# Optimization experiments

Hardware: AMD Instinct MI355X
Metric: run time of the kernel (lower is better)

Reference implementation:

```python
import jax, jax.numpy as jnp
import numpy as np

B, L, D, N_HEADS = 4, 8192, 1024, 16
HD = D // N_HEADS
MASK_NEG = -1e10


def setup_inputs() -> dict:
    key = jax.random.key(0)
    ks = jax.random.split(key, 5)
    # xavier_normal std for square Dense: sqrt(2/(fan_in+fan_out))
    std = (2.0 / (D + D)) ** 0.5
    return {
        "query": jax.random.normal(ks[0], (B, L, D), dtype=jnp.float32),
        "mask": jax.random.bernoulli(ks[1], 0.1, (B, L)),  # True = masked out
        "Wq": std * jax.random.normal(ks[2], (D, D), dtype=jnp.float32),
        "bq": jnp.zeros((D,), dtype=jnp.float32),
        "Wk": std * jax.random.normal(ks[3], (D, D), dtype=jnp.float32),
        "bk": jnp.zeros((D,), dtype=jnp.float32),
        "Wv": std * jax.random.normal(ks[4], (D, D), dtype=jnp.float32),
        "bv": jnp.zeros((D,), dtype=jnp.float32),
    }


def reference(query, mask, Wq, bq, Wk, bk, Wv, bv):
    # Self-attention: key = value = query (original falls back when key/value are None)
    q = query @ Wq + bq  # [B, L, D]
    k = query @ Wk + bk
    v = query @ Wv + bv
    # split heads: b l (n h) -> b l n h
    qs = q.reshape(B, L, N_HEADS, HD)
    ks_ = k.reshape(B, L, N_HEADS, HD)
    vs = v.reshape(B, L, N_HEADS, HD)
    m = mask[:, :, None, None]  # [B, L, 1, 1], broadcast over heads & dims
    K = jnp.where(m, MASK_NEG, ks_)
    V = jnp.where(m, 0.0, vs)
    # elu kernel feature map: phi(x) = elu(x) + 1 (elu(-1e10)+1 -> 0 for masked keys)
    phiK = jax.nn.elu(K) + 1.0
    phiQ = jax.nn.elu(qs) + 1.0
    # per-head kv summary: [B, N, HD_k, HD_v]
    kv = jnp.einsum('blnk,blnv->bnkv', phiK, V)
    # FAITHFUL to original einsum 'blk,bkv->blk': sums kv over v, elementwise with phiQ
    kv_sum = kv.sum(-1)  # [B, N, HD]
    out = phiQ * kv_sum[:, None, :, :]  # [B, L, N, HD]
    # combine heads: b l n h -> b l (n h)
    return out.reshape(B, L, D)
```

## Files before the change

### kernel.cpp

```cpp
#include <hip/hip_runtime.h>

typedef unsigned short u16;
typedef unsigned int u32;
typedef __attribute__((ext_vector_type(8))) short s16x8;
typedef __attribute__((ext_vector_type(4))) float f32x4;

#define GAS __attribute__((address_space(1)))
#define LAS __attribute__((address_space(3)))

#define BB 4
#define LL 8192
#define DD 1024
#define NH 16
#define HD 64
#define MROWS (BB * LL)
#define NWBT 2064

__device__ __forceinline__ u16 f2bf(float f) {
  u32 u = __builtin_bit_cast(u32, f);
  u32 r = (u + 0x7FFFu + ((u >> 16) & 1u)) >> 16;
  return (u16)r;
}
__device__ __forceinline__ float bf2f(u32 lo) {
  return __builtin_bit_cast(float, lo << 16);
}

__device__ __forceinline__ void async16(const void* g, void* l) {
  __builtin_amdgcn_global_load_lds((const GAS u32*)g, (LAS u32*)l, 16, 0, 0);
}

__device__ __forceinline__ bool get_mask(const void* mp, int row, int mode) {
  if (mode == 2) return ((const unsigned char*)mp)[row] != 0;
  if (mode == 1) return ((const float*)mp)[row] != 0.f;
  return ((const int*)mp)[row] != 0;
}

__global__ void build_wbt(const float* __restrict__ Wq, const float* __restrict__ Wk,
                          u16* __restrict__ WbT) {
  __shared__ float t[32][33];
  const int n0 = blockIdx.x * 32;
  const int k0 = blockIdx.y * 32;
  const float* W = (n0 >> 10) == 0 ? Wq : Wk;
  const int nloc = n0 & 1023;
  const int tx = threadIdx.x, ty = threadIdx.y;
#pragma unroll
  for (int j = 0; j < 32; j += 8)
    t[ty + j][tx] = W[(size_t)(k0 + ty + j) * DD + nloc + tx];
  __syncthreads();
#pragma unroll
  for (int j = 0; j < 32; j += 8)
    WbT[(size_t)(n0 + ty + j) * DD + k0 + tx] = f2bf(t[tx][ty + j]);
}

__global__ void build_aux(const float* __restrict__ Wv, const float* __restrict__ bq,
                          const float* __restrict__ bk, const float* __restrict__ bv,
                          const u32* __restrict__ m,
                          u16* __restrict__ WbT, float* __restrict__ bcat,
                          int* __restrict__ flag) {
  const int blk = blockIdx.x;
  const int tid = threadIdx.x;
  if (blk < 64) {
    int i = blk * 256 + tid;
    int k = i >> 4, h = i & 15;
    float s = 0.f;
    const float* p = Wv + (size_t)k * DD + h * HD;
#pragma unroll 8
    for (int j = 0; j < 64; ++j) s += p[j];
    WbT[(size_t)(2048 + h) * DD + k] = f2bf(s);
  } else if (blk < 73) {
    int i = (blk - 64) * 256 + tid;
    if (i < 1024) bcat[i] = bq[i];
    else if (i < 2048) bcat[i] = bk[i - 1024];
    else if (i < 2064) {
      float s = 0.f;
      const float* p = bv + (i - 2048) * HD;
#pragma unroll 8
      for (int j = 0; j < 64; ++j) s += p[j];
      bcat[i] = s;
    }
  } else {
    int i = (blk - 73) * 256 + tid;
    u32 v = m[i];
    int f = 0;
    if (v == 0x3F800000u) f = 1;
    else if (v > 1u) f = 2;
    if (f) atomicMax(flag, f);
  }
}

__global__ __launch_bounds__(256) void prep_q(
    const float* __restrict__ query, const u16* __restrict__ WbT,
    const float* __restrict__ bcat, const void* __restrict__ maskp,
    const int* __restrict__ mmode,
    u16* __restrict__ qb, float* __restrict__ sV) {
  __shared__ float sVp[2][16][16];
  const int tid = threadIdx.x;
  const int lane = tid & 63;
  const int w = tid >> 6;
  const int wl = w >> 1;
  const int ks = w & 1;
  const int l15 = lane & 15, l16 = lane >> 4;
  const int row0 = blockIdx.x * 32 + wl * 16;
  const int arow = row0 + l15;

  const float* qrow = query + (size_t)arow * DD + ks * 512 + l16 * 8;
  u16* qbrow = qb + (size_t)arow * DD + ks * 512 + l16 * 8;
  const u16* wrow = WbT + (size_t)(2048 + l15) * DD + ks * 512 + l16 * 8;

  f32x4 acc = {};
#pragma unroll
  for (int mac = 0; mac < 2; ++mac) {
    float4 qv[16];
    s16x8 wv[8];
#pragma unroll
    for (int s = 0; s < 8; ++s) {
      const int off = mac * 256 + s * 32;
      qv[s * 2] = *(const float4*)(qrow + off);
      qv[s * 2 + 1] = *(const float4*)(qrow + off + 4);
      wv[s] = *(const s16x8*)(wrow + off);
    }
#pragma unroll
    for (int s = 0; s < 8; ++s) {
      s16x8 o;
      o[0] = (short)f2bf(qv[s * 2].x);     o[1] = (short)f2bf(qv[s * 2].y);
      o[2] = (short)f2bf(qv[s * 2].z);     o[3] = (short)f2bf(qv[s * 2].w);
      o[4] = (short)f2bf(qv[s * 2 + 1].x); o[5] = (short)f2bf(qv[s * 2 + 1].y);
      o[6] = (short)f2bf(qv[s * 2 + 1].z); o[7] = (short)f2bf(qv[s * 2 + 1].w);
      *(s16x8*)(qbrow + mac * 256 + s * 32) = o;
      acc = __builtin_amdgcn_mfma_f32_16x16x32_bf16(o, wv[s], acc, 0, 0, 0);
    }
  }

  if (ks == 1) {
#pragma unroll
    for (int r = 0; r < 4; ++r) sVp[wl][l16 * 4 + r][l15] = acc[r];
  }
  __syncthreads();
  if (ks == 0) {
    const int mode = *mmode;
#pragma unroll
    for (int r = 0; r < 4; ++r) {
      const int row = row0 + l16 * 4 + r;
      const bool msk = get_mask(maskp, row, mode);
      float v = acc[r] + sVp[wl][l16 * 4 + r][l15] + bcat[2048 + l15];
      sV[(size_t)row * NH + l15] = msk ? 0.f : v;
    }
  }
}

#define AOFF(buf) ((buf) * 4096)
#define BOFF(buf) (8192 + (buf) * 16384)

__global__ __launch_bounds__(512, 2) void gemm_qkv(
    const u16* __restrict__ qb, const u16* __restrict__ WbT,
    const float* __restrict__ bcat, const void* __restrict__ maskp,
    const int* __restrict__ mmode,
    const float* __restrict__ sV, float* __restrict__ kv,
    float* __restrict__ out, int phase) {
  __shared__ __align__(16) u16 lds[40960];
  const int tid = threadIdx.x;
  const int lane = tid & 63;
  const int w = tid >> 6;
  const int wm = w & 1, wn = w >> 1;
  const int l15 = lane & 15, l16 = lane >> 4;

  const int bid = blockIdx.x;
  const int swz = (bid & 7) * 64 + (bid >> 3);
  const int mt = swz >> 1;
  const int nt = swz & 1;
  const int row0 = mt * 128;
  const int col0 = (phase ? 1024 : 0) + nt * 512;

  f32x4 acc[4][8] = {};

#define STAGE_A(buf, kt) do {                                               \
    int row_ = tid >> 2, slot_ = tid & 3;                                   \
    int c_ = slot_ ^ ((row_ >> 1) & 3);                                     \
    async16(qb + (size_t)(row0 + row_) * DD + (kt) * 32 + c_ * 8,           \
            lds + AOFF(buf) + tid * 8);                                     \
  } while (0)

#define STAGE_B(buf, kt) do {                                               \
    _Pragma("unroll")                                                       \
    for (int j_ = 0; j_ < 4; ++j_) {                                        \
      int li_ = tid + j_ * 512;                                             \
      int row_ = li_ >> 2, slot_ = li_ & 3;                                 \
      int c_ = slot_ ^ ((row_ >> 1) & 3);                                   \
      async16(WbT + (size_t)(col0 + row_) * DD + (kt) * 32 + c_ * 8,        \
              lds + BOFF(buf) + li_ * 8);                                   \
    }                                                                       \
  } while (0)

#define LDA(buf, a) do {                                                    \
    _Pragma("unroll")                                                       \
    for (int mi_ = 0; mi_ < 4; ++mi_) {                                     \
      int r_ = wm * 64 + mi_ * 16 + l15;                                    \
      a[mi_] = *(const s16x8*)(lds + AOFF(buf) + r_ * 32 +                  \
                               ((l16 ^ ((r_ >> 1) & 3)) * 8));              \
    }                                                                       \
  } while (0)

#define LDB4(buf, nb, b) do {                                               \
    _Pragma("unroll")                                                       \
    for (int q_ = 0; q_ < 4; ++q_) {                                        \
      int r_ = wn * 128 + (nb) * 64 + q_ * 16 + l15;                        \
      b[q_] = *(const s16x8*)(lds + BOFF(buf) + r_ * 32 +                   \
                              ((l16 ^ ((r_ >> 1) & 3)) * 8));               \
    }                                                                       \
  } while (0)

#define MM(a, b, nb) do {                                                   \
    __builtin_amdgcn_s_setprio(1);                                          \
    _Pragma("unroll")                                                       \
    for (int mi_ = 0; mi_ < 4; ++mi_) {                                     \
      _Pragma("unroll")                                                     \
      for (int q_ = 0; q_ < 4; ++q_) {                                      \
        acc[mi_][(nb)*4 + q_] = __builtin_amdgcn_mfma_f32_16x16x32_bf16(    \
            a[mi_], b[q_], acc[mi_][(nb)*4 + q_], 0, 0, 0);                 \
      }                                                                     \
    }                                                                       \
    __builtin_amdgcn_s_setprio(0);                                          \
  } while (0)

#define BAR() __builtin_amdgcn_s_barrier()
#define VMW1() asm volatile("s_waitcnt vmcnt(1)" ::: "memory")
#define VMW5() asm volatile("s_waitcnt vmcnt(5)" ::: "memory")
#define VMW0() asm volatile("s_waitcnt vmcnt(0)" ::: "memory")

  STAGE_A(0, 0); STAGE_B(0, 0); STAGE_A(1, 1); STAGE_B(1, 1);
  VMW5();
  BAR();

  for (int t = 0; t < 30; t += 2) {
    s16x8 a[4], b[4];
    LDA(0, a); LDB4(0, 0, b);
    if (t > 0) STAGE_B(1, t + 1);
    BAR(); MM(a, b, 0); BAR();
    LDB4(0, 1, b);
    STAGE_A(0, t + 2);
    BAR(); MM(a, b, 1); VMW1(); BAR();
    LDA(1, a); LDB4(1, 0, b);
    STAGE_B(0, t + 2);
    BAR(); MM(a, b, 0); BAR();
    LDB4(1, 1, b);
    STAGE_A(1, t + 3);
    BAR(); MM(a, b, 1); VMW1(); BAR();
  }

  {
    s16x8 a[4], b[4];
    LDA(0, a); LDB4(0, 0, b);
    STAGE_B(1, 31);
    BAR(); MM(a, b, 0); BAR();
    LDB4(0, 1, b);
    BAR(); MM(a, b, 1); VMW0(); BAR();
    LDA(1, a); LDB4(1, 0, b);
    BAR(); MM(a, b, 0); BAR();
    LDB4(1, 1, b);
    BAR(); MM(a, b, 1);
  }

  const int mode = *mmode;
  const int lanec = lane & 15, laneq = lane >> 4;
  const int wcol0 = col0 + wn * 128;
  const int b_ = row0 >> 13;

  if (phase == 1) {
    const int h0 = (wcol0 - 1024) >> 6;
    float pc[8] = {0.f, 0.f, 0.f, 0.f, 0.f, 0.f, 0.f, 0.f};
#pragma unroll
    for (int mi = 0; mi < 4; ++mi) {
#pragma unroll
      for (int r = 0; r < 4; ++r) {
        const int row = row0 + wm * 64 + mi * 16 + laneq * 4 + r;
        const bool msk = get_mask(maskp, row, mode);
        if (!msk) {
          const float sv0 = sV[(size_t)row * NH + h0];
          const float sv1 = sV[(size_t)row * NH + h0 + 1];
#pragma unroll
          for (int nj = 0; nj < 8; ++nj) {
            const int col = wcol0 + nj * 16 + lanec;
            float v = acc[mi][nj][r] + bcat[col];
            float phi = v > 0.f ? v + 1.f : __expf(v);
            pc[nj] += phi * (nj < 4 ? sv0 : sv1);
          }
        }
      }
    }
#pragma unroll
    for (int nj = 0; nj < 8; ++nj) {
      pc[nj] += __shfl_xor(pc[nj], 16);
      pc[nj] += __shfl_xor(pc[nj], 32);
    }
    if (laneq == 0) {
#pragma unroll
      for (int nj = 0; nj < 8; ++nj) {
        const int colk = wcol0 - 1024 + nj * 16 + lanec;
        atomicAdd(&kv[b_ * DD + colk], pc[nj]);
      }
    }
  } else {
    float kvv[8];
#pragma unroll
    for (int nj = 0; nj < 8; ++nj)
      kvv[nj] = kv[b_ * DD + wcol0 + nj * 16 + lanec];
#pragma unroll
    for (int mi = 0; mi < 4; ++mi) {
#pragma unroll
      for (int r = 0; r < 4; ++r) {
        const int row = row0 + wm * 64 + mi * 16 + laneq * 4 + r;
#pragma unroll
        for (int nj = 0; nj < 8; ++nj) {
          const int col = wcol0 + nj * 16 + lanec;
          float v = acc[mi][nj][r] + bcat[col];
          float phi = v > 0.f ? v + 1.f : __expf(v);
          out[(size_t)row * DD + col] = phi * kvv[nj];
        }
      }
    }
  }
}

extern "C" void kernel_launch(void* const* d_in, const int* in_sizes, int n_in,
                              void* d_out, int out_size, void* d_ws, size_t ws_size,
                              hipStream_t stream) {
  const float* query = (const float*)d_in[0];
  const void* maskp = d_in[1];
  const float* Wq = (const float*)d_in[2];
  const float* bq = (const float*)d_in[3];
  const float* Wk = (const float*)d_in[4];
  const float* bk = (const float*)d_in[5];
  const float* Wv = (const float*)d_in[6];
  const float* bv = (const float*)d_in[7];
  float* out = (float*)d_out;

  char* ws = (char*)d_ws;
  u16* qb = (u16*)ws;            ws += (size_t)MROWS * DD * 2;
  u16* WbT = (u16*)ws;           ws += (size_t)NWBT * DD * 2;
  float* sV = (float*)ws;        ws += (size_t)MROWS * NH * 4;
  float* bcat = (float*)ws;      ws += (size_t)NWBT * 4;
  float* kv = (float*)ws;        ws += (size_t)BB * DD * 4;
  int* mflag = (int*)ws;         ws += 256;

  hipMemsetAsync(kv, 0, (size_t)BB * DD * 4 + 256, stream);

  build_wbt<<<dim3(2048 / 32, DD / 32), dim3(32, 8), 0, stream>>>(Wq, Wk, WbT);
  build_aux<<<105, 256, 0, stream>>>(Wv, bq, bk, bv, (const u32*)maskp, WbT, bcat, mflag);
  prep_q<<<MROWS / 32, 256, 0, stream>>>(query, WbT, bcat, maskp, mflag, qb, sV);
  gemm_qkv<<<512, 512, 0, stream>>>(qb, WbT, bcat, maskp, mflag, sV, kv, out, 1);
  gemm_qkv<<<512, 512, 0, stream>>>(qb, WbT, bcat, maskp, mflag, sV, kv, out, 0);
}
```

Baseline: 416.7 us.

## Load GEMM A operand straight from global into registers, skipping LDS staging

The QKV GEMM no longer stages the activation (A) tile through shared memory. Each wave now loads its A fragments directly from global memory into registers, double-buffered as even and odd K-steps, while the weight (B) tile stays double-buffered in LDS. This removes the LDS A buffers and several barriers per iteration, shrinking LDS use from 80 KB to 64 KB per block and simplifying the schedule. In exchange, the four waves that share the same rows each fetch those A rows separately, so the same A data is read several times through the cache hierarchy, and global latency now sits on the register path feeding the MFMA instructions.

New measurement: 484.4 us. +16.3%, slower.

```diff
diff --git a/kernel.cpp b/kernel.cpp
--- a/kernel.cpp
+++ b/kernel.cpp
@@ -148,8 +148,7 @@
   }
 }
 
-#define AOFF(buf) ((buf) * 4096)
-#define BOFF(buf) (8192 + (buf) * 16384)
+#define BOFF(u) ((u) * 16384)
 
 __global__ __launch_bounds__(512, 2) void gemm_qkv(
     const u16* __restrict__ qb, const u16* __restrict__ WbT,
@@ -157,7 +156,7 @@
     const int* __restrict__ mmode,
     const float* __restrict__ sV, float* __restrict__ kv,
     float* __restrict__ out, int phase) {
-  __shared__ __align__(16) u16 lds[40960];
+  __shared__ __align__(16) u16 lds[32768];
   const int tid = threadIdx.x;
   const int lane = tid & 63;
   const int w = tid >> 6;
@@ -173,38 +172,30 @@
 
   f32x4 acc[4][8] = {};
 
-#define STAGE_A(buf, kt) do {                                               \
-    int row_ = tid >> 2, slot_ = tid & 3;                                   \
-    int c_ = slot_ ^ ((row_ >> 1) & 3);                                     \
-    async16(qb + (size_t)(row0 + row_) * DD + (kt) * 32 + c_ * 8,           \
-            lds + AOFF(buf) + tid * 8);                                     \
+  const u16* gA = qb + (size_t)(row0 + wm * 64 + l15) * DD + l16 * 8;
+
+#define LDAG(a, kt) do {                                                    \
+    _Pragma("unroll")                                                       \
+    for (int mi_ = 0; mi_ < 4; ++mi_)                                       \
+      a[mi_] = *(const s16x8*)(gA + (size_t)(mi_ * 16) * DD + (kt) * 32);   \
   } while (0)
 
-#define STAGE_B(buf, kt) do {                                               \
+#define STAGE_B(u, kt) do {                                                 \
     _Pragma("unroll")                                                       \
     for (int j_ = 0; j_ < 4; ++j_) {                                        \
       int li_ = tid + j_ * 512;                                             \
       int row_ = li_ >> 2, slot_ = li_ & 3;                                 \
       int c_ = slot_ ^ ((row_ >> 1) & 3);                                   \
       async16(WbT + (size_t)(col0 + row_) * DD + (kt) * 32 + c_ * 8,        \
-              lds + BOFF(buf) + li_ * 8);                                   \
+              lds + BOFF(u) + li_ * 8);                                     \
     }                                                                       \
   } while (0)
 
-#define LDA(buf, a) do {                                                    \
-    _Pragma("unroll")                                                       \
-    for (int mi_ = 0; mi_ < 4; ++mi_) {                                     \
-      int r_ = wm * 64 + mi_ * 16 + l15;                                    \
-      a[mi_] = *(const s16x8*)(lds + AOFF(buf) + r_ * 32 +                  \
-                               ((l16 ^ ((r_ >> 1) & 3)) * 8));              \
-    }                                                                       \
-  } while (0)
-
-#define LDB4(buf, nb, b) do {                                               \
+#define LDB4(u, nb, b) do {                                                 \
     _Pragma("unroll")                                                       \
     for (int q_ = 0; q_ < 4; ++q_) {                                        \
       int r_ = wn * 128 + (nb) * 64 + q_ * 16 + l15;                        \
-      b[q_] = *(const s16x8*)(lds + BOFF(buf) + r_ * 32 +                   \
+      b[q_] = *(const s16x8*)(lds + BOFF(u) + r_ * 32 +                     \
                               ((l16 ^ ((r_ >> 1) & 3)) * 8));               \
     }                                                                       \
   } while (0)
@@ -223,41 +214,26 @@
   } while (0)
 
 #define BAR() __builtin_amdgcn_s_barrier()
-#define VMW1() asm volatile("s_waitcnt vmcnt(1)" ::: "memory")
-#define VMW5() asm volatile("s_waitcnt vmcnt(5)" ::: "memory")
-#define VMW0() asm volatile("s_waitcnt vmcnt(0)" ::: "memory")
-
-  STAGE_A(0, 0); STAGE_B(0, 0); STAGE_A(1, 1); STAGE_B(1, 1);
-  VMW5();
+#define VMW(n) asm volatile("s_waitcnt vmcnt(" #n ")" ::: "memory")
+
+  s16x8 aE[4], aO[4];
+
+  STAGE_B(0, 0);
+  LDAG(aE, 0);
+  VMW(4);
   BAR();
 
-  for (int t = 0; t < 30; t += 2) {
-    s16x8 a[4], b[4];
-    LDA(0, a); LDB4(0, 0, b);
-    if (t > 0) STAGE_B(1, t + 1);
-    BAR(); MM(a, b, 0); BAR();
-    LDB4(0, 1, b);
-    STAGE_A(0, t + 2);
-    BAR(); MM(a, b, 1); VMW1(); BAR();
-    LDA(1, a); LDB4(1, 0, b);
-    STAGE_B(0, t + 2);
-    BAR(); MM(a, b, 0); BAR();
-    LDB4(1, 1, b);
-    STAGE_A(1, t + 3);
-    BAR(); MM(a, b, 1); VMW1(); BAR();
-  }
-
-  {
-    s16x8 a[4], b[4];
-    LDA(0, a); LDB4(0, 0, b);
-    STAGE_B(1, 31);
-    BAR(); MM(a, b, 0); BAR();
-    LDB4(0, 1, b);
-    BAR(); MM(a, b, 1); VMW0(); BAR();
-    LDA(1, a); LDB4(1, 0, b);
-    BAR(); MM(a, b, 0); BAR();
-    LDB4(1, 1, b);
-    BAR(); MM(a, b, 1);
+  for (int t = 0; t < 32; t += 2) {
+    s16x8 b[4];
+    STAGE_B(1, t + 1);
+    LDAG(aO, t + 1);
+    LDB4(0, 0, b); MM(aE, b, 0);
+    LDB4(0, 1, b); MM(aE, b, 1);
+    VMW(4); BAR();
+    if (t < 30) { STAGE_B(0, t + 2); LDAG(aE, t + 2); }
+    LDB4(1, 0, b); MM(aO, b, 0);
+    LDB4(1, 1, b); MM(aO, b, 1);
+    if (t < 30) { VMW(4); BAR(); }
   }
 
   const int mode = *mmode;
```
